# Performance work log

Hardware: AMD Instinct MI355X
Metric: run time of the kernel (lower is better)

Reference implementation:

```python
import jax, jax.numpy as jnp
import numpy as np

DIM = 1024
H = 16
HD = DIM // H          # head_dim = 64
SCALE = HD ** -0.5
LAMBDA_INIT = 0.1


def setup_inputs() -> dict:
    key = jax.random.key(0)
    ks = jax.random.split(key, 8)
    B, NQ, NKV = 4, 1024, 1024
    # xavier_uniform for linear weights; stored as (in, out) for x @ W
    def xavier(k, fan_in, fan_out):
        a = float(np.sqrt(6.0 / (fan_in + fan_out)))
        return jax.random.uniform(k, (fan_in, fan_out), jnp.float32, -a, a)
    return {
        "DriftData": jax.random.normal(ks[0], (B, NQ, DIM), jnp.float32),
        "OceanData": jax.random.normal(ks[1], (B, NKV, DIM), jnp.float32),
        "Wq": xavier(ks[2], DIM, 2 * DIM),
        "Wk": xavier(ks[3], DIM, 2 * DIM),
        "Wv": xavier(ks[4], DIM, DIM),
        "Wo": xavier(ks[5], DIM, DIM),
        "lambda_q1": jax.random.normal(ks[6], (H, HD), jnp.float32),
        "lambda_k1": jax.random.normal(jax.random.fold_in(ks[6], 1), (H, HD), jnp.float32),
        "lambda_q2": jax.random.normal(ks[7], (H, HD), jnp.float32),
        "lambda_k2": jax.random.normal(jax.random.fold_in(ks[7], 1), (H, HD), jnp.float32),
    }


def reference(DriftData, OceanData, Wq, Wk, Wv, Wo,
              lambda_q1, lambda_k1, lambda_q2, lambda_k2):
    B, NQ, dim = DriftData.shape
    NKV = OceanData.shape[1]
    # lambda scalar per head: exp(q1.k1) - exp(q2.k2) + lambda_init  -> (H,)
    lam = (jnp.exp(jnp.sum(lambda_q1 * lambda_k1, axis=-1))
           - jnp.exp(jnp.sum(lambda_q2 * lambda_k2, axis=-1)) + LAMBDA_INIT)
    # projections: Q,K -> 2*dim, V -> dim
    Q = (DriftData @ Wq).reshape(B, NQ, H, 2 * HD).transpose(0, 2, 1, 3)   # b h q 2hd
    K = (OceanData @ Wk).reshape(B, NKV, H, 2 * HD).transpose(0, 2, 1, 3)  # b h k 2hd
    V = (OceanData @ Wv).reshape(B, NKV, H, HD).transpose(0, 2, 1, 3)      # b h k hd
    Q1, Q2 = Q[..., :HD], Q[..., HD:]
    K1, K2 = K[..., :HD], K[..., HD:]
    A1 = jnp.einsum('bhqd,bhkd->bhqk', Q1, K1) * SCALE
    A2 = jnp.einsum('bhqd,bhkd->bhqk', Q2, K2) * SCALE
    att = jax.nn.softmax(A1, axis=-1) - lam[None, :, None, None] * jax.nn.softmax(A2, axis=-1)
    out = jnp.einsum('bhqk,bhkd->bhqd', att, V)            # b h q hd
    out = out.transpose(0, 2, 1, 3).reshape(B, NQ, dim)    # b q dim
    return out @ Wo
```

## Files before the change

kernel.cpp:

```cpp
#include <hip/hip_runtime.h>
#include <hip/hip_bf16.h>

typedef unsigned short u16;
typedef unsigned int u32;
typedef __attribute__((ext_vector_type(8))) short short8;
typedef __attribute__((ext_vector_type(4))) float f32x4;
typedef __attribute__((ext_vector_type(4))) u16 us4;

#define MFMA16(a,b,c) __builtin_amdgcn_mfma_f32_16x16x32_bf16(a,b,c,0,0,0)

__device__ __forceinline__ u16 f2b(float x){
  u32 u = __builtin_bit_cast(u32, x);
  u32 r = (u + 0x7fffu + ((u >> 16) & 1u)) >> 16;
  return (u16)r;
}
__device__ __forceinline__ u16 f2b_hw(float x){
  return __builtin_bit_cast(u16, __float2bfloat16(x));
}
__device__ __forceinline__ float ex2(float x){ return __builtin_amdgcn_exp2f(x); }

__device__ __forceinline__ void gll16(const u16* g, u16* l){
  __builtin_amdgcn_global_load_lds((const __attribute__((address_space(1))) u32*)g,
                                   (__attribute__((address_space(3))) u32*)l, 16, 0, 0);
}

__global__ __launch_bounds__(256) void k_conv2(const float* __restrict__ a, const float* __restrict__ bsrc,
                                               u16* __restrict__ ya, u16* __restrict__ yb){
  int bid = blockIdx.x;
  const float* x = (bid < 4096) ? a : bsrc;
  u16* y = (bid < 4096) ? ya : yb;
  int i = (bid & 4095) * 256 + threadIdx.x;
  float4 v = reinterpret_cast<const float4*>(x)[i];
  us4 o; o.x = f2b(v.x); o.y = f2b(v.y); o.z = f2b(v.z); o.w = f2b(v.w);
  reinterpret_cast<us4*>(y)[i] = o;
}

__global__ __launch_bounds__(256) void k_prep_w(const float* __restrict__ Wq, const float* __restrict__ Wk,
                                                const float* __restrict__ Wv, const float* __restrict__ Wo,
                                                u16* __restrict__ WqT, u16* __restrict__ WkvT,
                                                u16* __restrict__ WoT,
                                                const float* __restrict__ lq1, const float* __restrict__ lk1,
                                                const float* __restrict__ lq2, const float* __restrict__ lk2,
                                                float* __restrict__ lam){
  __shared__ float t[32][33];
  const int z = blockIdx.z;
  const float* W; u16* WT; int N; float scale = 1.0f;
  if (z == 0){ W = Wq; WT = WqT; N = 2048; scale = 0.1803368867f; }
  else if (z == 1){ W = Wk; WT = WkvT; N = 2048; }
  else if (z == 2){ W = Wv; WT = WkvT + 2048*1024; N = 1024; }
  else { W = Wo; WT = WoT; N = 1024; }
  int n0 = blockIdx.x * 32, k0 = blockIdx.y * 32;
  int tx = threadIdx.x & 31, ty = threadIdx.x >> 5;
  if (n0 < N){
    #pragma unroll
    for (int i = 0; i < 4; i++)
      t[ty + i*8][tx] = W[(size_t)(k0 + ty + i*8) * N + n0 + tx];
    __syncthreads();
    #pragma unroll
    for (int i = 0; i < 4; i++)
      WT[(size_t)(n0 + ty + i*8) * 1024 + k0 + tx] = f2b(t[tx][ty + i*8] * scale);
  }
  if (z == 3 && blockIdx.x == 0 && blockIdx.y == 0 && threadIdx.x < 16){
    int h = threadIdx.x;
    float d1 = 0.f, d2 = 0.f;
    for (int i = 0; i < 64; i++){
      d1 += lq1[h*64 + i] * lk1[h*64 + i];
      d2 += lq2[h*64 + i] * lk2[h*64 + i];
    }
    lam[h] = expf(d1) - expf(d2) + 0.1f;
  }
}

__global__ __launch_bounds__(256) void k_transpose_v(const u16* __restrict__ KV, u16* __restrict__ VT){
  __shared__ u16 t[32][34];
  int kv0 = blockIdx.x * 32, d0 = blockIdx.y * 32, bh = blockIdx.z;
  int b = bh >> 4, h = bh & 15;
  int tx = threadIdx.x & 31, ty = threadIdx.x >> 5;
  #pragma unroll
  for (int i = 0; i < 4; i++)
    t[ty + i*8][tx] = KV[(size_t)(b*1024 + kv0 + ty + i*8) * 3072 + 2048 + h*64 + d0 + tx];
  __syncthreads();
  #pragma unroll
  for (int i = 0; i < 4; i++)
    VT[(size_t)bh * 65536 + (size_t)(d0 + ty + i*8) * 1024 + kv0 + tx] = t[tx][ty + i*8];
}

template<bool OUTF32>
__device__ __forceinline__ void gemm_body(const u16* __restrict__ A, const u16* __restrict__ B,
                                          void* __restrict__ C, int N, int m0, int n0,
                                          u16* As, u16* Bs){
  const int tid = threadIdx.x;
  const int wave = tid >> 6, lane = tid & 63;
  const int lr = lane & 15, lg = lane >> 4;
  const int wm = wave >> 1, wn = wave & 1;

  f32x4 acc[4][4];
  #pragma unroll
  for (int i = 0; i < 4; i++)
    #pragma unroll
    for (int j = 0; j < 4; j++){ f32x4 z = {0.f,0.f,0.f,0.f}; acc[i][j] = z; }

  const int srow = tid >> 3;
  const int skc  = tid & 7;

  for (int k0 = 0; k0 < 1024; k0 += 64){
    #pragma unroll
    for (int c = 0; c < 4; c++){
      int row = c*32 + srow;
      const u16* ga = A + (size_t)(m0 + row) * 1024 + k0 + ((skc ^ (row & 7)) << 3);
      gll16(ga, As + c*2048 + wave*512);
      const u16* gb = B + (size_t)(n0 + row) * 1024 + k0 + ((skc ^ (row & 7)) << 3);
      gll16(gb, Bs + c*2048 + wave*512);
    }
    __syncthreads();
    #pragma unroll
    for (int kc = 0; kc < 2; kc++){
      short8 af[4], bfr[4];
      #pragma unroll
      for (int mt = 0; mt < 4; mt++){
        int row = wm*64 + mt*16 + lr;
        af[mt] = *reinterpret_cast<const short8*>(As + row*64 + (((kc*4 + lg) ^ (row & 7)) << 3));
      }
      #pragma unroll
      for (int nt = 0; nt < 4; nt++){
        int rown = wn*64 + nt*16 + lr;
        bfr[nt] = *reinterpret_cast<const short8*>(Bs + rown*64 + (((kc*4 + lg) ^ (rown & 7)) << 3));
      }
      #pragma unroll
      for (int mt = 0; mt < 4; mt++)
        #pragma unroll
        for (int nt = 0; nt < 4; nt++)
          acc[mt][nt] = MFMA16(af[mt], bfr[nt], acc[mt][nt]);
    }
    __syncthreads();
  }
  #pragma unroll
  for (int mt = 0; mt < 4; mt++)
    #pragma unroll
    for (int nt = 0; nt < 4; nt++)
      #pragma unroll
      for (int r = 0; r < 4; r++){
        int row = m0 + wm*64 + mt*16 + lg*4 + r;
        int col = n0 + wn*64 + nt*16 + lr;
        if (OUTF32) ((float*)C)[(size_t)row * N + col] = acc[mt][nt][r];
        else        ((u16*)C)[(size_t)row * N + col] = f2b(acc[mt][nt][r]);
      }
}

__global__ __launch_bounds__(256) void k_gemm_proj(const u16* __restrict__ Xd, const u16* __restrict__ Xo,
                                                   const u16* __restrict__ WqT, const u16* __restrict__ WkvT,
                                                   u16* __restrict__ Qb, u16* __restrict__ KVb){
  __shared__ __align__(16) u16 As[128*64];
  __shared__ __align__(16) u16 Bs[128*64];
  int bid0 = blockIdx.x;
  int bid = (bid0 & 7) * 160 + (bid0 >> 3);
  if (bid < 512){
    gemm_body<false>(Xd, WqT, Qb, 2048, (bid >> 4) * 128, (bid & 15) * 128, As, Bs);
  } else {
    int t = bid - 512;
    gemm_body<false>(Xo, WkvT, KVb, 3072, (t / 24) * 128, (t % 24) * 128, As, Bs);
  }
}

__global__ __launch_bounds__(256) void k_gemm_out(const u16* __restrict__ A, const u16* __restrict__ B,
                                                  float* __restrict__ C){
  __shared__ __align__(16) u16 As[128*64];
  __shared__ __align__(16) u16 Bs[128*64];
  int bid = blockIdx.x;
  gemm_body<true>(A, B, C, 1024, (bid >> 3) * 128, (bid & 7) * 128, As, Bs);
}

__device__ __forceinline__ void softmax_t(f32x4 s[4], float& l, u16* pl, int lr, int lg){
  float sum = 0.f;
  #pragma unroll
  for (int nt = 0; nt < 4; nt++)
    #pragma unroll
    for (int r = 0; r < 4; r++){
      float p = ex2(s[nt][r]);
      s[nt][r] = p;
      sum += p;
    }
  sum += __shfl_xor(sum, 16);
  sum += __shfl_xor(sum, 32);
  l += sum;
  char* base = (char*)pl + lr * 128;
  const int swz = (lr & 7) << 4;
  #pragma unroll
  for (int nt = 0; nt < 4; nt++){
    us4 h;
    h.x = f2b_hw(s[nt][0]); h.y = f2b_hw(s[nt][1]);
    h.z = f2b_hw(s[nt][2]); h.w = f2b_hw(s[nt][3]);
    *reinterpret_cast<us4*>(base + ((nt*32 + lg*8) ^ swz)) = h;
  }
}

__global__ __launch_bounds__(256, 2) void k_attn(const u16* __restrict__ Q, const u16* __restrict__ KVb,
                                                 const u16* __restrict__ VT, const float* __restrict__ lam,
                                                 u16* __restrict__ O){
  int bid = blockIdx.x;
  int logical = (bid & 7) * 64 + (bid >> 3);
  int qt8 = logical & 7, h = (logical >> 3) & 15, b = logical >> 7;
  const int tid = threadIdx.x, wave = tid >> 6, lane = tid & 63;
  const int lr = lane & 15, lg = lane >> 4;
  const int qb = qt8 * 128 + wave * 32;

  __shared__ __align__(16) u16 Ks[2][8192];
  __shared__ __align__(16) u16 Vs[2][4096];
  __shared__ __align__(16) u16 Pl[4][2][2][1024];

  const int srow = tid >> 4, schunk = tid & 15;
  const int vrow = tid >> 3, vchunk = tid & 7;
  const u16* Kg = KVb + (size_t)(b*1024 + srow) * 3072 + h*128 + ((schunk ^ (srow & 7)) << 3);
  const u16* Vg = VT + (size_t)(b*16 + h) * 65536 + (size_t)vrow * 1024 + ((vchunk ^ (vrow & 7)) << 3);

  short8 qf[2][2][2];
  #pragma unroll
  for (int qt = 0; qt < 2; qt++){
    const u16* Qp = Q + (size_t)(b*1024 + qb + qt*16 + lr) * 2048 + h*128 + lg*8;
    #pragma unroll
    for (int kc = 0; kc < 2; kc++){
      qf[0][qt][kc] = *reinterpret_cast<const short8*>(Qp + kc*32);
      qf[1][qt][kc] = *reinterpret_cast<const short8*>(Qp + 64 + kc*32);
    }
  }
  const float lamh = lam[h];

  f32x4 o[2][4][2];
  #pragma unroll
  for (int br = 0; br < 2; br++)
    #pragma unroll
    for (int nt = 0; nt < 4; nt++)
      #pragma unroll
      for (int qt = 0; qt < 2; qt++){ f32x4 z = {0.f,0.f,0.f,0.f}; o[br][nt][qt] = z; }
  float l[2][2] = {{0.f, 0.f}, {0.f, 0.f}};

  auto STAGE = [&](int buf, int kv0){
    u16* kd = &Ks[buf][tid * 8];
    #pragma unroll
    for (int i = 0; i < 4; i++)
      gll16(Kg + (size_t)(kv0 + i*16) * 3072, kd + i*2048);
    u16* vd = &Vs[buf][tid * 8];
    #pragma unroll
    for (int j = 0; j < 2; j++)
      gll16(Vg + kv0 + (size_t)(j*32) * 1024, vd + j*2048);
  };

  STAGE(0, 0);
  __syncthreads();

  for (int t = 0; t < 16; t++){
    const int cur = t & 1;
    if (t < 15) STAGE(cur ^ 1, (t + 1) << 6);

    const u16* kbuf = &Ks[cur][0];
    const u16* vbuf = &Vs[cur][0];

    #pragma unroll
    for (int br = 0; br < 2; br++){
      short8 kf[4][2];
      #pragma unroll
      for (int nt = 0; nt < 4; nt++)
        #pragma unroll
        for (int kc = 0; kc < 2; kc++)
          kf[nt][kc] = *reinterpret_cast<const short8*>(
              kbuf + (nt*16 + lr)*128 + (((br*8 + kc*4 + lg) ^ (lr & 7)) << 3));
      #pragma unroll
      for (int qt = 0; qt < 2; qt++){
        f32x4 s[4];
        #pragma unroll
        for (int nt = 0; nt < 4; nt++){ f32x4 z = {0.f,0.f,0.f,0.f}; s[nt] = z; }
        __builtin_amdgcn_s_setprio(1);
        #pragma unroll
        for (int nt = 0; nt < 4; nt++)
          #pragma unroll
          for (int kc = 0; kc < 2; kc++)
            s[nt] = MFMA16(kf[nt][kc], qf[br][qt][kc], s[nt]);
        __builtin_amdgcn_s_setprio(0);
        softmax_t(s, l[br][qt], &Pl[wave][qt][br][0], lr, lg);
      }
    }

    const int swz = (lr & 7) << 4;
    __builtin_amdgcn_s_setprio(1);
    #pragma unroll
    for (int kc = 0; kc < 2; kc++){
      short8 pf[2][2];
      #pragma unroll
      for (int qt = 0; qt < 2; qt++)
        #pragma unroll
        for (int br = 0; br < 2; br++)
          pf[qt][br] = *reinterpret_cast<const short8*>(
              (char*)&Pl[wave][qt][br][0] + lr*128 + ((kc*64 + lg*16) ^ swz));
      #pragma unroll
      for (int nt = 0; nt < 4; nt++){
        short8 vf = *reinterpret_cast<const short8*>(
            vbuf + (nt*16 + lr)*64 + (((kc*4 + lg) ^ (lr & 7)) << 3));
        #pragma unroll
        for (int qt = 0; qt < 2; qt++){
          o[0][nt][qt] = MFMA16(vf, pf[qt][0], o[0][nt][qt]);
          o[1][nt][qt] = MFMA16(vf, pf[qt][1], o[1][nt][qt]);
        }
      }
    }
    __builtin_amdgcn_s_setprio(0);
    __syncthreads();
  }

  #pragma unroll
  for (int qt = 0; qt < 2; qt++){
    const float inv1 = 1.0f / l[0][qt];
    const float inv2 = lamh / l[1][qt];
    u16* Op = O + (size_t)(b*1024 + qb + qt*16 + lr) * 1024 + h*64;
    #pragma unroll
    for (int nt = 0; nt < 4; nt++){
      us4 hh;
      #pragma unroll
      for (int r = 0; r < 4; r++){
        float v = o[0][nt][qt][r] * inv1 - o[1][nt][qt][r] * inv2;
        ((u16*)&hh)[r] = f2b_hw(v);
      }
      *reinterpret_cast<us4*>(Op + nt*16 + lg*4) = hh;
    }
  }
}

extern "C" void kernel_launch(void* const* d_in, const int* in_sizes, int n_in,
                              void* d_out, int out_size, void* d_ws, size_t ws_size,
                              hipStream_t stream){
  const float* Drift = (const float*)d_in[0];
  const float* Ocean = (const float*)d_in[1];
  const float* Wq    = (const float*)d_in[2];
  const float* Wk    = (const float*)d_in[3];
  const float* Wv    = (const float*)d_in[4];
  const float* Wo    = (const float*)d_in[5];
  const float* lq1   = (const float*)d_in[6];
  const float* lk1   = (const float*)d_in[7];
  const float* lq2   = (const float*)d_in[8];
  const float* lk2   = (const float*)d_in[9];
  float* out = (float*)d_out;

  char* ws = (char*)d_ws;
  u16* Xd   = (u16*)(ws);
  u16* Xo   = (u16*)(ws + 8388608);
  u16* WqT  = (u16*)(ws + 16777216);
  u16* WkvT = (u16*)(ws + 20971520);
  u16* WoT  = (u16*)(ws + 27262976);
  u16* Qb   = (u16*)(ws + 29360128);
  u16* KVb  = (u16*)(ws + 46137344);
  u16* VTb  = (u16*)(ws + 71303168);
  u16* Ob   = (u16*)(ws + 79691776);
  float* lam = (float*)(ws + 88080384);

  k_conv2<<<8192, 256, 0, stream>>>(Drift, Ocean, Xd, Xo);
  k_prep_w<<<dim3(64,32,4), 256, 0, stream>>>(Wq, Wk, Wv, Wo, WqT, WkvT, WoT,
                                              lq1, lk1, lq2, lk2, lam);
  k_gemm_proj<<<1280, 256, 0, stream>>>(Xd, Xo, WqT, WkvT, Qb, KVb);
  k_transpose_v<<<dim3(32,2,64), 256, 0, stream>>>(KVb, VTb);
  k_attn<<<512, 256, 0, stream>>>(Qb, KVb, VTb, lam, Ob);
  k_gemm_out<<<256, 256, 0, stream>>>(Ob, WoT, out);
}
```

Baseline: 144.5 us.

## Widen attention blocks to 8 waves sharing K/V tiles; merge prep kernels

The attention kernel now runs 512-thread blocks covering 256 queries per (batch, head), so each staged K/V tile in LDS is reused by twice as many waves. Each thread issues fewer async global-to-LDS loads per stage, and the P staging buffer doubles to fit. This is meant to halve redundant K/V global reads, at the cost of more LDS per block and fewer, larger blocks on the grid. Separately, the input conversion and weight transpose/prep kernels are folded into one launch to save a kernel launch.

```diff
diff --git a/kernel.cpp b/kernel.cpp
--- a/kernel.cpp
+++ b/kernel.cpp
@@ -24,32 +24,35 @@
                                    (__attribute__((address_space(3))) u32*)l, 16, 0, 0);
 }
 
-__global__ __launch_bounds__(256) void k_conv2(const float* __restrict__ a, const float* __restrict__ bsrc,
-                                               u16* __restrict__ ya, u16* __restrict__ yb){
+__global__ __launch_bounds__(256) void k_prep(const float* __restrict__ Drift, const float* __restrict__ Ocean,
+                                              const float* __restrict__ Wq, const float* __restrict__ Wk,
+                                              const float* __restrict__ Wv, const float* __restrict__ Wo,
+                                              u16* __restrict__ Xd, u16* __restrict__ Xo,
+                                              u16* __restrict__ WqT, u16* __restrict__ WkvT,
+                                              u16* __restrict__ WoT,
+                                              const float* __restrict__ lq1, const float* __restrict__ lk1,
+                                              const float* __restrict__ lq2, const float* __restrict__ lk2,
+                                              float* __restrict__ lam){
+  __shared__ float t[32][33];
   int bid = blockIdx.x;
-  const float* x = (bid < 4096) ? a : bsrc;
-  u16* y = (bid < 4096) ? ya : yb;
-  int i = (bid & 4095) * 256 + threadIdx.x;
-  float4 v = reinterpret_cast<const float4*>(x)[i];
-  us4 o; o.x = f2b(v.x); o.y = f2b(v.y); o.z = f2b(v.z); o.w = f2b(v.w);
-  reinterpret_cast<us4*>(y)[i] = o;
-}
-
-__global__ __launch_bounds__(256) void k_prep_w(const float* __restrict__ Wq, const float* __restrict__ Wk,
-                                                const float* __restrict__ Wv, const float* __restrict__ Wo,
-                                                u16* __restrict__ WqT, u16* __restrict__ WkvT,
-                                                u16* __restrict__ WoT,
-                                                const float* __restrict__ lq1, const float* __restrict__ lk1,
-                                                const float* __restrict__ lq2, const float* __restrict__ lk2,
-                                                float* __restrict__ lam){
-  __shared__ float t[32][33];
-  const int z = blockIdx.z;
+  if (bid < 8192){
+    const float* x = (bid < 4096) ? Drift : Ocean;
+    u16* y = (bid < 4096) ? Xd : Xo;
+    int i = (bid & 4095) * 256 + threadIdx.x;
+    float4 v = reinterpret_cast<const float4*>(x)[i];
+    us4 o; o.x = f2b(v.x); o.y = f2b(v.y); o.z = f2b(v.z); o.w = f2b(v.w);
+    reinterpret_cast<us4*>(y)[i] = o;
+    return;
+  }
+  int tt = bid - 8192;
+  int z = tt >> 11;
+  int bx = tt & 63, by = (tt & 2047) >> 6;
   const float* W; u16* WT; int N; float scale = 1.0f;
   if (z == 0){ W = Wq; WT = WqT; N = 2048; scale = 0.1803368867f; }
   else if (z == 1){ W = Wk; WT = WkvT; N = 2048; }
   else if (z == 2){ W = Wv; WT = WkvT + 2048*1024; N = 1024; }
   else { W = Wo; WT = WoT; N = 1024; }
-  int n0 = blockIdx.x * 32, k0 = blockIdx.y * 32;
+  int n0 = bx * 32, k0 = by * 32;
   int tx = threadIdx.x & 31, ty = threadIdx.x >> 5;
   if (n0 < N){
     #pragma unroll
@@ -60,7 +63,7 @@
     for (int i = 0; i < 4; i++)
       WT[(size_t)(n0 + ty + i*8) * 1024 + k0 + tx] = f2b(t[tx][ty + i*8] * scale);
   }
-  if (z == 3 && blockIdx.x == 0 && blockIdx.y == 0 && threadIdx.x < 16){
+  if (z == 3 && bx == 0 && by == 0 && threadIdx.x < 16){
     int h = threadIdx.x;
     float d1 = 0.f, d2 = 0.f;
     for (int i = 0; i < 64; i++){
@@ -194,19 +197,19 @@
   }
 }
 
-__global__ __launch_bounds__(256, 2) void k_attn(const u16* __restrict__ Q, const u16* __restrict__ KVb,
-                                                 const u16* __restrict__ VT, const float* __restrict__ lam,
-                                                 u16* __restrict__ O){
+__global__ __launch_bounds__(512) void k_attn(const u16* __restrict__ Q, const u16* __restrict__ KVb,
+                                              const u16* __restrict__ VT, const float* __restrict__ lam,
+                                              u16* __restrict__ O){
   int bid = blockIdx.x;
-  int logical = (bid & 7) * 64 + (bid >> 3);
-  int qt8 = logical & 7, h = (logical >> 3) & 15, b = logical >> 7;
+  int logical = (bid & 7) * 32 + (bid >> 3);
+  int qt2 = logical & 3, h = (logical >> 2) & 15, b = logical >> 6;
   const int tid = threadIdx.x, wave = tid >> 6, lane = tid & 63;
   const int lr = lane & 15, lg = lane >> 4;
-  const int qb = qt8 * 128 + wave * 32;
+  const int qb = qt2 * 256 + wave * 32;
 
   __shared__ __align__(16) u16 Ks[2][8192];
   __shared__ __align__(16) u16 Vs[2][4096];
-  __shared__ __align__(16) u16 Pl[4][2][2][1024];
+  __shared__ __align__(16) u16 Pl[8][2][2][1024];
 
   const int srow = tid >> 4, schunk = tid & 15;
   const int vrow = tid >> 3, vchunk = tid & 7;
@@ -235,14 +238,10 @@
   float l[2][2] = {{0.f, 0.f}, {0.f, 0.f}};
 
   auto STAGE = [&](int buf, int kv0){
-    u16* kd = &Ks[buf][tid * 8];
-    #pragma unroll
-    for (int i = 0; i < 4; i++)
-      gll16(Kg + (size_t)(kv0 + i*16) * 3072, kd + i*2048);
-    u16* vd = &Vs[buf][tid * 8];
-    #pragma unroll
-    for (int j = 0; j < 2; j++)
-      gll16(Vg + kv0 + (size_t)(j*32) * 1024, vd + j*2048);
+    #pragma unroll
+    for (int i = 0; i < 2; i++)
+      gll16(Kg + (size_t)(kv0 + i*32) * 3072, &Ks[buf][i*4096 + tid*8]);
+    gll16(Vg + kv0, &Vs[buf][tid*8]);
   };
 
   STAGE(0, 0);
@@ -351,11 +350,10 @@
   u16* Ob   = (u16*)(ws + 79691776);
   float* lam = (float*)(ws + 88080384);
 
-  k_conv2<<<8192, 256, 0, stream>>>(Drift, Ocean, Xd, Xo);
-  k_prep_w<<<dim3(64,32,4), 256, 0, stream>>>(Wq, Wk, Wv, Wo, WqT, WkvT, WoT,
-                                              lq1, lk1, lq2, lk2, lam);
+  k_prep<<<16384, 256, 0, stream>>>(Drift, Ocean, Wq, Wk, Wv, Wo, Xd, Xo,
+                                    WqT, WkvT, WoT, lq1, lk1, lq2, lk2, lam);
   k_gemm_proj<<<1280, 256, 0, stream>>>(Xd, Xo, WqT, WkvT, Qb, KVb);
   k_transpose_v<<<dim3(32,2,64), 256, 0, stream>>>(KVb, VTb);
-  k_attn<<<512, 256, 0, stream>>>(Qb, KVb, VTb, lam, Ob);
+  k_attn<<<256, 512, 0, stream>>>(Qb, KVb, VTb, lam, Ob);
   k_gemm_out<<<256, 256, 0, stream>>>(Ob, WoT, out);
 }
```

Result: no change. 143.2 us (-0.9%).
